# Kernel tuning notes

Hardware: AMD Instinct MI355X
Metric: run time of the kernel (lower is better)

The kernel has to match this reference:

```python
import jax, jax.numpy as jnp
import numpy as np

H, W = 128, 128
K = 16                # num_samples
RADIUS = 2.0
SIGMA = 1.0
EPS = 1e-10
MIN_DEPTH = 1e-6
N = 16384             # number of points
FEAT_DIM = 64
FAR = 1e9             # sentinel pixel coord for invalid (behind-camera) points


def setup_inputs() -> dict:
    key = jax.random.key(0)
    k1, k2, k3, k4, k5 = jax.random.split(key, 5)
    fx = fy = 128.0
    cx = cy = 64.0
    # Back-project uniform pixel locations with z in [1, 5] so points land on the image.
    u = jax.random.uniform(k1, (N,), minval=0.0, maxval=float(W))
    v = jax.random.uniform(k2, (N,), minval=0.0, maxval=float(H))
    z = jax.random.uniform(k3, (N,), minval=1.0, maxval=5.0)
    x = (u - cx) * z / fx
    y = (v - cy) * z / fy
    pcd_points = jnp.stack([x, y, z], axis=-1).astype(jnp.float32)
    pcd_colors = jax.random.uniform(k4, (N, 3), dtype=jnp.float32)
    pcd_feats = jax.random.normal(k5, (N, FEAT_DIM), dtype=jnp.float32)
    intrinsics = jnp.array([[fx, 0.0, cx], [0.0, fy, cy], [0.0, 0.0, 1.0]], dtype=jnp.float32)
    return {"pcd_points": pcd_points, "pcd_colors": pcd_colors,
            "pcd_feats": pcd_feats, "intrinsics": intrinsics}


def _render_pixels(pcd_points, intrinsics):
    # Project to pixel coords (u, v); points behind camera pushed to FAR so kNN never picks them.
    depths = pcd_points[:, 2]
    valid = depths > MIN_DEPTH
    safe_z = jnp.where(valid, depths, 1.0)
    u = pcd_points[:, 0] * intrinsics[0, 0] / safe_z + intrinsics[0, 2]
    v = pcd_points[:, 1] * intrinsics[1, 1] / safe_z + intrinsics[1, 2]
    pix = jnp.stack([u, v], axis=-1)                       # (N, 2)
    pix = jnp.where(valid[:, None], pix, FAR)
    return pix, depths


def _forward(pcd_points, pcd_colors, pcd_feats, intrinsics):
    pix, depths = _render_pixels(pcd_points, intrinsics)
    # Centered pixel grid, row-major flatten: coords are (x+0.5, y+0.5).
    ii, jj = jnp.meshgrid(jnp.arange(H), jnp.arange(W), indexing='ij')
    img_pix = jnp.stack([jj.ravel() + 0.5, ii.ravel() + 0.5], axis=-1).astype(pix.dtype)  # (P, 2)
    # Brute-force 2D kNN: (P, N) squared distances. Indices are non-differentiable.
    d2 = jnp.sum((img_pix[:, None, :] - pix[None, :, :]) ** 2, axis=-1)  # (P, N)
    _, idx = jax.lax.top_k(-jax.lax.stop_gradient(d2), K)                # (P, K)
    # Depth-sort the k neighbors (ascending), as torch.sort on zbuffers.
    zbuf = depths[idx]
    order = jnp.argsort(zbuf, axis=-1)
    idx = jnp.take_along_axis(idx, order, axis=-1)                       # (P, K)
    # Distances of sorted neighbors to the pixel center (differentiable path).
    knn_pix = pix[idx]                                                   # (P, K, 2)
    dist = jnp.linalg.norm(knn_pix - img_pix[:, None, :], axis=-1)       # (P, K)
    masks = dist < RADIUS
    # Exponential weighting + weighted (normalized) compositing.
    w = jnp.exp(-(dist ** 2) / (SIGMA ** 2)) * masks.astype(dist.dtype)
    w = w / (jnp.sum(w, axis=-1, keepdims=True) + EPS)
    sel_depths = depths[idx]                                             # (P, K)
    rendered_depths = jnp.sum(sel_depths * w, axis=-1).reshape(H, W)
    rendered_colors = jnp.sum(pcd_colors[idx] * w[..., None], axis=1).reshape(H, W, 3)
    rendered_feats = jnp.sum(pcd_feats[idx] * w[..., None], axis=1).reshape(H, W, FEAT_DIM)
    rendered_masks = jnp.any(masks, axis=-1).reshape(H, W)
    return rendered_depths, rendered_colors, rendered_feats, rendered_masks


def reference(pcd_points, pcd_colors, pcd_feats, intrinsics):
    return _forward(pcd_points, pcd_colors, pcd_feats, intrinsics)
```

## Files before the change

### kernel.cpp

```cpp
#include <hip/hip_runtime.h>

#define HH 128
#define WW 128
#define HW 16384
#define KK 16
#define NPTS 16384
#define FEAT 64
#define RADIUS2 4.0f
#define EPSV 1e-10f

__global__ void project_kernel(const float* __restrict__ pts,
                               const float* __restrict__ intr,
                               float4* __restrict__ puvdi,
                               int* __restrict__ cell_of,
                               int* __restrict__ cell_count) {
    int n = blockIdx.x * blockDim.x + threadIdx.x;
    if (n >= NPTS) return;
    float fx = intr[0], cx = intr[2], fy = intr[4], cy = intr[5];
    float x = pts[3 * n], y = pts[3 * n + 1], z = pts[3 * n + 2];
    bool valid = z > 1e-6f;
    float sz = valid ? z : 1.0f;
    float u = x * fx / sz + cx;
    float v = y * fy / sz + cy;
    if (!valid) { u = 1e9f; v = 1e9f; }
    puvdi[n] = make_float4(u, v, z, __int_as_float(n));
    int cell = -1;
    if (valid) {
        int cu = (int)floorf(u); cu = min(max(cu, 0), WW - 1);
        int cv = (int)floorf(v); cv = min(max(cv, 0), HH - 1);
        cell = cv * WW + cu;
        atomicAdd(&cell_count[cell], 1);
    }
    cell_of[n] = cell;
}

__global__ __launch_bounds__(256) void scan_kernel(const int4* __restrict__ count4,
                                                   int* __restrict__ start,
                                                   int* __restrict__ cursor) {
    __shared__ int wsum_s[4];
    int tid = threadIdx.x;
    int4 c[16];
#pragma unroll
    for (int q = 0; q < 16; ++q) c[q] = count4[tid * 16 + q];
    int s = 0;
#pragma unroll
    for (int q = 0; q < 16; ++q) s += c[q].x + c[q].y + c[q].z + c[q].w;
    int lane = tid & 63, wv = tid >> 6;
    int incl = s;
#pragma unroll
    for (int d = 1; d < 64; d <<= 1) {
        int t = __shfl_up(incl, d, 64);
        if (lane >= d) incl += t;
    }
    if (lane == 63) wsum_s[wv] = incl;
    __syncthreads();
    int wbase = 0;
#pragma unroll
    for (int q = 0; q < 4; ++q) wbase += (q < wv) ? wsum_s[q] : 0;
    int acc = wbase + incl - s;
    int base = tid * 64;
#pragma unroll
    for (int q = 0; q < 16; ++q) {
        int4 st;
        st.x = acc; acc += c[q].x;
        st.y = acc; acc += c[q].y;
        st.z = acc; acc += c[q].z;
        st.w = acc; acc += c[q].w;
        ((int4*)(start + base))[q] = st;
        ((int4*)(cursor + base))[q] = st;
    }
    if (tid == 255) start[HW] = acc;
}

__global__ void scatter_kernel(const float4* __restrict__ puvdi,
                               const int* __restrict__ cell_of,
                               int* __restrict__ cursor,
                               float4* __restrict__ suvdi) {
    int n = blockIdx.x * blockDim.x + threadIdx.x;
    if (n >= NPTS) return;
    int cell = cell_of[n];
    if (cell < 0) return;
    int pos = atomicAdd(&cursor[cell], 1);
    suvdi[pos] = puvdi[n];
}

__global__ __launch_bounds__(64) void render_kernel(
        const float4* __restrict__ suvdi,
        const int* __restrict__ start,
        const float* __restrict__ colors,
        float* __restrict__ out_depth, float* __restrict__ out_colors,
        float* __restrict__ out_mask,
        int* __restrict__ knn_idx, float* __restrict__ knn_w) {
    __shared__ float4 pts_s[1024];
    __shared__ int S[8][13];
    __shared__ int row_off[9];

    int tid = threadIdx.x;
    int tile = blockIdx.x;
    int j0 = (tile & 15) * 8;
    int i0 = (tile >> 4) * 4;

    for (int idx = tid; idx < 104; idx += 64) {
        int r = idx / 13, c = idx - r * 13;
        int ci = i0 - 2 + r;
        int col = min(max(j0 - 2 + c, 0), 128);
        int v = 0;
        if (ci >= 0 && ci < HH) v = start[ci * WW + col];
        S[r][c] = v;
    }
    __syncthreads();
    if (tid == 0) {
        int acc = 0;
#pragma unroll
        for (int r = 0; r < 8; ++r) { row_off[r] = acc; acc += S[r][12] - S[r][0]; }
        row_off[8] = acc;
    }
    __syncthreads();
    int T = min(row_off[8], 1024);

    for (int idx = tid; idx < T; idx += 64) {
        int r = 0;
#pragma unroll
        for (int q = 1; q < 8; ++q) r = (idx >= row_off[q]) ? q : r;
        int g = S[r][0] + (idx - row_off[r]);
        pts_s[idx] = suvdi[g];
    }
    __syncthreads();

    int lp = tid >> 1, lane = tid & 1;
    int li = lp >> 3, lj = lp & 7;
    int i = i0 + li, j = j0 + lj;
    int p = i * WW + j;
    float px = j + 0.5f, py = i + 0.5f;
    int ca = max(j - 2, 0) - (j0 - 2);
    int cb = min(j + 2, WW - 1) + 1 - (j0 - 2);

    float bd[KK];
    int   bt[KK];
#pragma unroll
    for (int k = 0; k < KK; ++k) { bd[k] = 1e30f; bt[k] = -1; }

#pragma unroll
    for (int dr = 0; dr < 5; ++dr) {
        int r = li + dr;
        int g0 = S[r][ca], g1 = S[r][cb];
        int base = row_off[r] - S[r][0];
        for (int g = g0 + lane; g < g1; g += 2) {
            float4 pt = pts_s[base + g];
            float du = pt.x - px, dv = pt.y - py;
            float d2 = du * du + dv * dv;
            bool ok = d2 < RADIUS2;
            float dd = ok ? d2 : 1e30f;
            int tt = ok ? (base + g) : -1;
#pragma unroll
            for (int k = 0; k < KK; ++k) {
                bool cc = dd < bd[k];
                float nb = cc ? dd : bd[k];
                dd = cc ? bd[k] : dd;
                int nt = cc ? tt : bt[k];
                tt = cc ? bt[k] : tt;
                bd[k] = nb; bt[k] = nt;
            }
        }
    }

    float mb[8]; int mt[8];
#pragma unroll
    for (int k = 0; k < 8; ++k) {
        float obd = __shfl_xor(bd[15 - k], 1);
        int   obt = __shfl_xor(bt[15 - k], 1);
        bool take = obd < bd[k];
        mb[k] = take ? obd : bd[k];
        mt[k] = take ? obt : bt[k];
    }

    float wv[8], dv8[8];
    int idv[8];
    float wsum_l = 0.f;
    int any_l = 0;
#pragma unroll
    for (int k = 0; k < 8; ++k) {
        bool valid = mt[k] >= 0;
        float4 pt = pts_s[valid ? mt[k] : 0];
        float wk = valid ? __expf(-mb[k]) : 0.f;
        wv[k] = wk; wsum_l += wk;
        dv8[k] = valid ? pt.z : 0.f;
        idv[k] = valid ? __float_as_int(pt.w) : -1;
        any_l |= valid ? 1 : 0;
    }
    float wsum = wsum_l + __shfl_xor(wsum_l, 1);
    float inv = 1.0f / (wsum + EPSV);

    float cr[8], cg[8], cbl[8];
#pragma unroll
    for (int k = 0; k < 8; ++k) {
        int n3 = idv[k] >= 0 ? 3 * idv[k] : 0;
        cr[k] = colors[n3];
        cg[k] = colors[n3 + 1];
        cbl[k] = colors[n3 + 2];
    }

    float dsum = 0.f, c0 = 0.f, c1 = 0.f, c2 = 0.f;
    int   io[8]; float wo[8];
#pragma unroll
    for (int k = 0; k < 8; ++k) {
        float wk = wv[k] * inv;
        io[k] = idv[k];
        wo[k] = wk;
        dsum += dv8[k] * wk;
        c0 += cr[k] * wk;
        c1 += cg[k] * wk;
        c2 += cbl[k] * wk;
    }

    int4*   ki4 = (int4*)(knn_idx + p * KK + lane * 8);
    float4* kw4 = (float4*)(knn_w + p * KK + lane * 8);
    ki4[0] = make_int4(io[0], io[1], io[2], io[3]);
    ki4[1] = make_int4(io[4], io[5], io[6], io[7]);
    kw4[0] = make_float4(wo[0], wo[1], wo[2], wo[3]);
    kw4[1] = make_float4(wo[4], wo[5], wo[6], wo[7]);

    dsum += __shfl_xor(dsum, 1);
    c0 += __shfl_xor(c0, 1);
    c1 += __shfl_xor(c1, 1);
    c2 += __shfl_xor(c2, 1);
    any_l |= __shfl_xor(any_l, 1);

    if (lane == 0) {
        out_depth[p] = dsum;
        out_colors[3 * p]     = c0;
        out_colors[3 * p + 1] = c1;
        out_colors[3 * p + 2] = c2;
        out_mask[p] = any_l ? 1.0f : 0.0f;
    }
}

__global__ void feats_kernel(const float* __restrict__ feats,
                             const int* __restrict__ knn_idx,
                             const float* __restrict__ knn_w,
                             float* __restrict__ out_feats) {
    int p = blockIdx.x * blockDim.y + threadIdx.y;
    int f = threadIdx.x;
    int nn[KK]; float wk[KK];
#pragma unroll
    for (int k = 0; k < KK; ++k) {
        nn[k] = knn_idx[p * KK + k];
        wk[k] = knn_w[p * KK + k];
    }
    float fv[KK];
#pragma unroll
    for (int k = 0; k < KK; ++k) {
        int n = nn[k] >= 0 ? nn[k] : 0;
        fv[k] = feats[n * FEAT + f];
    }
    float acc = 0.f;
#pragma unroll
    for (int k = 0; k < KK; ++k) {
        float m = nn[k] >= 0 ? wk[k] : 0.f;
        acc += m * fv[k];
    }
    out_feats[p * FEAT + f] = acc;
}

extern "C" void kernel_launch(void* const* d_in, const int* in_sizes, int n_in,
                              void* d_out, int out_size, void* d_ws, size_t ws_size,
                              hipStream_t stream) {
    const float* pts    = (const float*)d_in[0];
    const float* colors = (const float*)d_in[1];
    const float* feats  = (const float*)d_in[2];
    const float* intr   = (const float*)d_in[3];

    float* out = (float*)d_out;
    float* out_depth  = out;
    float* out_colors = out + HW;
    float* out_feats  = out + HW * 4;
    float* out_mask   = out + HW * 68;

    const size_t SLOT = 16448;
    char* ws = (char*)d_ws;
    float4* puvdi   = (float4*)(ws + 0 * SLOT * 4);
    int* cell_of    = (int*)   (ws + 4 * SLOT * 4);
    int* cell_count = (int*)   (ws + 5 * SLOT * 4);
    int* start      = (int*)   (ws + 6 * SLOT * 4);
    int* cursor     = (int*)   (ws + 7 * SLOT * 4);
    float4* suvdi   = (float4*)(ws + 8 * SLOT * 4);
    int* knn_idx    = (int*)   (ws + 12 * SLOT * 4);
    float* knn_w    = (float*) (ws + 12 * SLOT * 4 + HW * KK * 4);

    hipMemsetAsync(cell_count, 0, HW * sizeof(int), stream);

    project_kernel<<<NPTS / 256, 256, 0, stream>>>(pts, intr, puvdi, cell_of, cell_count);
    scan_kernel<<<1, 256, 0, stream>>>((const int4*)cell_count, start, cursor);
    scatter_kernel<<<NPTS / 256, 256, 0, stream>>>(puvdi, cell_of, cursor, suvdi);
    render_kernel<<<512, 64, 0, stream>>>(suvdi, start, colors,
                                          out_depth, out_colors, out_mask, knn_idx, knn_w);
    dim3 fb(FEAT, 4);
    feats_kernel<<<HW / 4, fb, 0, stream>>>(feats, knn_idx, knn_w, out_feats);
}
```

Measured before the change: 99.27 us.

## Replace counting sort with fixed-capacity cell buckets and fuse feature gather into render

Drops the scan and scatter kernels. Points are written directly into per-cell fixed-capacity buckets (CAP=16) during projection. The feature-gather kernel is folded into the render kernel, with the kNN indices and weights staged in shared memory instead of round-tripping through global workspace. This cuts the launch count from five kernels to two and removes intermediate global traffic. In exchange, cells holding more than 16 points silently drop points, and each 64-thread render block now does the full 64-dim feature gather for its 32 pixels.

```diff
diff --git a/kernel.cpp b/kernel.cpp
--- a/kernel.cpp
+++ b/kernel.cpp
@@ -8,12 +8,12 @@
 #define FEAT 64
 #define RADIUS2 4.0f
 #define EPSV 1e-10f
-
-__global__ void project_kernel(const float* __restrict__ pts,
-                               const float* __restrict__ intr,
-                               float4* __restrict__ puvdi,
-                               int* __restrict__ cell_of,
-                               int* __restrict__ cell_count) {
+#define CAP 16
+
+__global__ void project_scatter(const float* __restrict__ pts,
+                                const float* __restrict__ intr,
+                                int* __restrict__ cell_count,
+                                float4* __restrict__ buckets) {
     int n = blockIdx.x * blockDim.x + threadIdx.x;
     if (n >= NPTS) return;
     float fx = intr[0], cx = intr[2], fy = intr[4], cy = intr[5];
@@ -22,108 +22,54 @@
     float sz = valid ? z : 1.0f;
     float u = x * fx / sz + cx;
     float v = y * fy / sz + cy;
-    if (!valid) { u = 1e9f; v = 1e9f; }
-    puvdi[n] = make_float4(u, v, z, __int_as_float(n));
-    int cell = -1;
-    if (valid) {
-        int cu = (int)floorf(u); cu = min(max(cu, 0), WW - 1);
-        int cv = (int)floorf(v); cv = min(max(cv, 0), HH - 1);
-        cell = cv * WW + cu;
-        atomicAdd(&cell_count[cell], 1);
-    }
-    cell_of[n] = cell;
+    if (!valid) return;
+    int cu = min(max((int)floorf(u), 0), WW - 1);
+    int cv = min(max((int)floorf(v), 0), HH - 1);
+    int cell = cv * WW + cu;
+    int slot = atomicAdd(&cell_count[cell], 1);
+    if (slot < CAP)
+        buckets[slot * HW + cell] = make_float4(u, v, z, __int_as_float(n));
 }
 
-__global__ __launch_bounds__(256) void scan_kernel(const int4* __restrict__ count4,
-                                                   int* __restrict__ start,
-                                                   int* __restrict__ cursor) {
-    __shared__ int wsum_s[4];
-    int tid = threadIdx.x;
-    int4 c[16];
-#pragma unroll
-    for (int q = 0; q < 16; ++q) c[q] = count4[tid * 16 + q];
-    int s = 0;
-#pragma unroll
-    for (int q = 0; q < 16; ++q) s += c[q].x + c[q].y + c[q].z + c[q].w;
-    int lane = tid & 63, wv = tid >> 6;
-    int incl = s;
-#pragma unroll
-    for (int d = 1; d < 64; d <<= 1) {
-        int t = __shfl_up(incl, d, 64);
-        if (lane >= d) incl += t;
-    }
-    if (lane == 63) wsum_s[wv] = incl;
-    __syncthreads();
-    int wbase = 0;
-#pragma unroll
-    for (int q = 0; q < 4; ++q) wbase += (q < wv) ? wsum_s[q] : 0;
-    int acc = wbase + incl - s;
-    int base = tid * 64;
-#pragma unroll
-    for (int q = 0; q < 16; ++q) {
-        int4 st;
-        st.x = acc; acc += c[q].x;
-        st.y = acc; acc += c[q].y;
-        st.z = acc; acc += c[q].z;
-        st.w = acc; acc += c[q].w;
-        ((int4*)(start + base))[q] = st;
-        ((int4*)(cursor + base))[q] = st;
-    }
-    if (tid == 255) start[HW] = acc;
-}
-
-__global__ void scatter_kernel(const float4* __restrict__ puvdi,
-                               const int* __restrict__ cell_of,
-                               int* __restrict__ cursor,
-                               float4* __restrict__ suvdi) {
-    int n = blockIdx.x * blockDim.x + threadIdx.x;
-    if (n >= NPTS) return;
-    int cell = cell_of[n];
-    if (cell < 0) return;
-    int pos = atomicAdd(&cursor[cell], 1);
-    suvdi[pos] = puvdi[n];
-}
-
 __global__ __launch_bounds__(64) void render_kernel(
-        const float4* __restrict__ suvdi,
-        const int* __restrict__ start,
+        const float4* __restrict__ buckets,
+        const int* __restrict__ cell_count,
         const float* __restrict__ colors,
+        const float* __restrict__ feats,
         float* __restrict__ out_depth, float* __restrict__ out_colors,
-        float* __restrict__ out_mask,
-        int* __restrict__ knn_idx, float* __restrict__ knn_w) {
-    __shared__ float4 pts_s[1024];
-    __shared__ int S[8][13];
-    __shared__ int row_off[9];
+        float* __restrict__ out_feats, float* __restrict__ out_mask) {
+    __shared__ float4 pts_s[CAP * 96];
+    __shared__ int    cnt_s[96];
+    __shared__ float  knw_s[32][KK];
+    __shared__ int    kni_s[32][KK];
 
     int tid = threadIdx.x;
     int tile = blockIdx.x;
     int j0 = (tile & 15) * 8;
     int i0 = (tile >> 4) * 4;
 
-    for (int idx = tid; idx < 104; idx += 64) {
-        int r = idx / 13, c = idx - r * 13;
-        int ci = i0 - 2 + r;
-        int col = min(max(j0 - 2 + c, 0), 128);
-        int v = 0;
-        if (ci >= 0 && ci < HH) v = start[ci * WW + col];
-        S[r][c] = v;
-    }
+    int mymax = 0;
+    for (int idx = tid; idx < 96; idx += 64) {
+        int r = idx / 12, c = idx - r * 12;
+        int ci = i0 - 2 + r, cj = j0 - 2 + c;
+        int cnt = 0;
+        if (ci >= 0 && ci < HH && cj >= 0 && cj < WW)
+            cnt = min(cell_count[ci * WW + cj], CAP);
+        cnt_s[idx] = cnt;
+        mymax = max(mymax, cnt);
+    }
+#pragma unroll
+    for (int d = 32; d; d >>= 1) mymax = max(mymax, __shfl_xor(mymax, d));
+    int M = mymax;
     __syncthreads();
-    if (tid == 0) {
-        int acc = 0;
-#pragma unroll
-        for (int r = 0; r < 8; ++r) { row_off[r] = acc; acc += S[r][12] - S[r][0]; }
-        row_off[8] = acc;
-    }
-    __syncthreads();
-    int T = min(row_off[8], 1024);
-
-    for (int idx = tid; idx < T; idx += 64) {
-        int r = 0;
-#pragma unroll
-        for (int q = 1; q < 8; ++q) r = (idx >= row_off[q]) ? q : r;
-        int g = S[r][0] + (idx - row_off[r]);
-        pts_s[idx] = suvdi[g];
+
+    for (int s = 0; s < M; ++s) {
+        for (int idx = tid; idx < 96; idx += 64) {
+            int r = idx / 12, c = idx - r * 12;
+            int ci = i0 - 2 + r, cj = j0 - 2 + c;
+            if (s < cnt_s[idx])
+                pts_s[s * 96 + idx] = buckets[s * HW + ci * WW + cj];
+        }
     }
     __syncthreads();
 
@@ -132,8 +78,6 @@
     int i = i0 + li, j = j0 + lj;
     int p = i * WW + j;
     float px = j + 0.5f, py = i + 0.5f;
-    int ca = max(j - 2, 0) - (j0 - 2);
-    int cb = min(j + 2, WW - 1) + 1 - (j0 - 2);
 
     float bd[KK];
     int   bt[KK];
@@ -143,23 +87,27 @@
 #pragma unroll
     for (int dr = 0; dr < 5; ++dr) {
         int r = li + dr;
-        int g0 = S[r][ca], g1 = S[r][cb];
-        int base = row_off[r] - S[r][0];
-        for (int g = g0 + lane; g < g1; g += 2) {
-            float4 pt = pts_s[base + g];
-            float du = pt.x - px, dv = pt.y - py;
-            float d2 = du * du + dv * dv;
-            bool ok = d2 < RADIUS2;
-            float dd = ok ? d2 : 1e30f;
-            int tt = ok ? (base + g) : -1;
-#pragma unroll
-            for (int k = 0; k < KK; ++k) {
-                bool cc = dd < bd[k];
-                float nb = cc ? dd : bd[k];
-                dd = cc ? bd[k] : dd;
-                int nt = cc ? tt : bt[k];
-                tt = cc ? bt[k] : tt;
-                bd[k] = nb; bt[k] = nt;
+#pragma unroll
+        for (int dc = 0; dc < 5; ++dc) {
+            int c = lj + dc;
+            int wc = r * 12 + c;
+            int cnt = cnt_s[wc];
+            for (int s = lane; s < cnt; s += 2) {
+                float4 pt = pts_s[s * 96 + wc];
+                float du = pt.x - px, dv = pt.y - py;
+                float d2 = du * du + dv * dv;
+                bool ok = d2 < RADIUS2;
+                float dd = ok ? d2 : 1e30f;
+                int tt = ok ? (s * 96 + wc) : -1;
+#pragma unroll
+                for (int k = 0; k < KK; ++k) {
+                    bool cc = dd < bd[k];
+                    float nb = cc ? dd : bd[k];
+                    dd = cc ? bd[k] : dd;
+                    int nt = cc ? tt : bt[k];
+                    tt = cc ? bt[k] : tt;
+                    bd[k] = nb; bt[k] = nt;
+                }
             }
         }
     }
@@ -201,24 +149,16 @@
     }
 
     float dsum = 0.f, c0 = 0.f, c1 = 0.f, c2 = 0.f;
-    int   io[8]; float wo[8];
 #pragma unroll
     for (int k = 0; k < 8; ++k) {
         float wk = wv[k] * inv;
-        io[k] = idv[k];
-        wo[k] = wk;
+        kni_s[lp][lane * 8 + k] = idv[k];
+        knw_s[lp][lane * 8 + k] = wk;
         dsum += dv8[k] * wk;
         c0 += cr[k] * wk;
         c1 += cg[k] * wk;
         c2 += cbl[k] * wk;
     }
-
-    int4*   ki4 = (int4*)(knn_idx + p * KK + lane * 8);
-    float4* kw4 = (float4*)(knn_w + p * KK + lane * 8);
-    ki4[0] = make_int4(io[0], io[1], io[2], io[3]);
-    ki4[1] = make_int4(io[4], io[5], io[6], io[7]);
-    kw4[0] = make_float4(wo[0], wo[1], wo[2], wo[3]);
-    kw4[1] = make_float4(wo[4], wo[5], wo[6], wo[7]);
 
     dsum += __shfl_xor(dsum, 1);
     c0 += __shfl_xor(c0, 1);
@@ -233,33 +173,27 @@
         out_colors[3 * p + 2] = c2;
         out_mask[p] = any_l ? 1.0f : 0.0f;
     }
-}
-
-__global__ void feats_kernel(const float* __restrict__ feats,
-                             const int* __restrict__ knn_idx,
-                             const float* __restrict__ knn_w,
-                             float* __restrict__ out_feats) {
-    int p = blockIdx.x * blockDim.y + threadIdx.y;
-    int f = threadIdx.x;
-    int nn[KK]; float wk[KK];
-#pragma unroll
-    for (int k = 0; k < KK; ++k) {
-        nn[k] = knn_idx[p * KK + k];
-        wk[k] = knn_w[p * KK + k];
-    }
-    float fv[KK];
-#pragma unroll
-    for (int k = 0; k < KK; ++k) {
-        int n = nn[k] >= 0 ? nn[k] : 0;
-        fv[k] = feats[n * FEAT + f];
-    }
-    float acc = 0.f;
-#pragma unroll
-    for (int k = 0; k < KK; ++k) {
-        float m = nn[k] >= 0 ? wk[k] : 0.f;
-        acc += m * fv[k];
-    }
-    out_feats[p * FEAT + f] = acc;
+    __syncthreads();
+
+    int f = tid;
+    for (int q = 0; q < 32; q += 2) {
+        float acc0 = 0.f, acc1 = 0.f;
+#pragma unroll
+        for (int k = 0; k < KK; ++k) {
+            int n0 = kni_s[q][k];
+            int n1 = kni_s[q + 1][k];
+            float w0 = knw_s[q][k];
+            float w1 = knw_s[q + 1][k];
+            float f0 = feats[(n0 >= 0 ? n0 : 0) * FEAT + f];
+            float f1 = feats[(n1 >= 0 ? n1 : 0) * FEAT + f];
+            acc0 = fmaf(w0, f0, acc0);
+            acc1 = fmaf(w1, f1, acc1);
+        }
+        int p0 = (i0 + (q >> 3)) * WW + j0 + (q & 7);
+        int p1 = (i0 + ((q + 1) >> 3)) * WW + j0 + ((q + 1) & 7);
+        out_feats[p0 * FEAT + f] = acc0;
+        out_feats[p1 * FEAT + f] = acc1;
+    }
 }
 
 extern "C" void kernel_launch(void* const* d_in, const int* in_sizes, int n_in,
@@ -276,24 +210,12 @@
     float* out_feats  = out + HW * 4;
     float* out_mask   = out + HW * 68;
 
-    const size_t SLOT = 16448;
     char* ws = (char*)d_ws;
-    float4* puvdi   = (float4*)(ws + 0 * SLOT * 4);
-    int* cell_of    = (int*)   (ws + 4 * SLOT * 4);
-    int* cell_count = (int*)   (ws + 5 * SLOT * 4);
-    int* start      = (int*)   (ws + 6 * SLOT * 4);
-    int* cursor     = (int*)   (ws + 7 * SLOT * 4);
-    float4* suvdi   = (float4*)(ws + 8 * SLOT * 4);
-    int* knn_idx    = (int*)   (ws + 12 * SLOT * 4);
-    float* knn_w    = (float*) (ws + 12 * SLOT * 4 + HW * KK * 4);
+    int* cell_count  = (int*)ws;
+    float4* buckets  = (float4*)(ws + HW * sizeof(int));
 
     hipMemsetAsync(cell_count, 0, HW * sizeof(int), stream);
-
-    project_kernel<<<NPTS / 256, 256, 0, stream>>>(pts, intr, puvdi, cell_of, cell_count);
-    scan_kernel<<<1, 256, 0, stream>>>((const int4*)cell_count, start, cursor);
-    scatter_kernel<<<NPTS / 256, 256, 0, stream>>>(puvdi, cell_of, cursor, suvdi);
-    render_kernel<<<512, 64, 0, stream>>>(suvdi, start, colors,
-                                          out_depth, out_colors, out_mask, knn_idx, knn_w);
-    dim3 fb(FEAT, 4);
-    feats_kernel<<<HW / 4, fb, 0, stream>>>(feats, knn_idx, knn_w, out_feats);
+    project_scatter<<<NPTS / 256, 256, 0, stream>>>(pts, intr, cell_count, buckets);
+    render_kernel<<<512, 64, 0, stream>>>(buckets, cell_count, colors, feats,
+                                          out_depth, out_colors, out_feats, out_mask);
 }
```

Result: slower. 106.3 us (+7.1%).
